# Kernel tuning notes

Hardware: AMD Instinct MI355X
Metric: run time of the kernel (lower is better)

The kernel has to match this reference:

```python
import jax, jax.numpy as jnp
import numpy as np

N_STATES = 35
EMIT_SCALE = -500.0


def _constants():
    prior = jnp.full((N_STATES,), -10.0, dtype=jnp.float32).at[0].set(10.0)
    eye = jnp.eye(N_STATES, dtype=jnp.float32)
    trans = (0.1 * eye
             + 0.8 * jnp.roll(eye, 1, axis=1)
             + 0.08 * jnp.roll(eye, 2, axis=1)
             + (0.02 / N_STATES) * jnp.ones((N_STATES, N_STATES), dtype=jnp.float32))
    # Categorical(probs=trans).logits == log of row-normalized probs
    log_trans = jnp.log(trans / trans.sum(axis=-1, keepdims=True))
    return prior, log_trans


def setup_inputs() -> dict:
    key = jax.random.key(0)
    k1, k2 = jax.random.split(key)
    observations = jax.random.normal(k1, (64, 512, 16, 13, 12), dtype=jnp.float32)
    obs_matrix = jax.random.uniform(k2, (35, 16, 13, 12), dtype=jnp.float32)
    return {"observations": observations, "obs_matrix": obs_matrix}


def reference(observations, obs_matrix):
    prior, log_trans = _constants()
    B, T = observations.shape[:2]
    D = 16 * 13 * 12  # flattened frame dim = 2496
    x = observations.reshape(B, T, D)           # [B,T,D]
    m = obs_matrix.reshape(N_STATES, D)         # [S,D]
    x_sq = jnp.sum(x * x, axis=-1)              # [B,T]
    m_sq = jnp.sum(m * m, axis=-1)              # [S]
    xm = jnp.einsum('btd,sd->bts', x, m)        # [B,T,S]
    emis = (x_sq[..., None] + m_sq[None, None, :] - 2.0 * xm) / EMIT_SCALE  # [B,T,S]

    alpha0 = emis[:, 0] + prior                 # [B,S]
    log_trans_T = log_trans.T                   # [j,i] -> logT[i,j]

    def step(alpha, e_t):
        # alpha'[b,j] = e_t[b,j] + LSE_i(logT[i,j] + alpha[b,i])
        new = e_t + jax.nn.logsumexp(log_trans_T[None, :, :] + alpha[:, None, :], axis=2)
        return new, None

    emis_rest = jnp.swapaxes(emis[:, 1:], 0, 1)  # [T-1,B,S]
    alpha, _ = jax.lax.scan(step, alpha0, emis_rest)
    return jax.nn.logsumexp(alpha, axis=1)       # [B]
```

## Files before the change

### kernel.cpp

```cpp
#include <hip/hip_runtime.h>


#define ROWS 32768
#define KD   2496
#define NS   35
#define SPAD 48
#define ES   40
#define TT   512

typedef short v8s __attribute__((ext_vector_type(8)));
typedef float v4f __attribute__((ext_vector_type(4)));

__device__ __forceinline__ unsigned short f2bf(float f) {
    unsigned u = __builtin_bit_cast(unsigned, f);
    u += 0x7fffu + ((u >> 16) & 1u);
    return (unsigned short)(u >> 16);
}

template <int CTRL, int RM>
__device__ __forceinline__ float dppf(float oldv, float v) {
    return __builtin_bit_cast(float, __builtin_amdgcn_update_dpp(
        __builtin_bit_cast(int, oldv), __builtin_bit_cast(int, v),
        CTRL, RM, 0xf, false));
}

__device__ __forceinline__ float wsum63(float v) {
    v += dppf<0x111, 0xf>(0.f, v);
    v += dppf<0x112, 0xf>(0.f, v);
    v += dppf<0x114, 0xf>(0.f, v);
    v += dppf<0x118, 0xf>(0.f, v);
    v += dppf<0x142, 0xa>(0.f, v);
    v += dppf<0x143, 0xc>(0.f, v);
    return __builtin_bit_cast(float,
        __builtin_amdgcn_readlane(__builtin_bit_cast(int, v), 63));
}

__device__ __forceinline__ float wmax63(float v) {
    const float NI = -3.0e38f;
    v = fmaxf(v, dppf<0x111, 0xf>(NI, v));
    v = fmaxf(v, dppf<0x112, 0xf>(NI, v));
    v = fmaxf(v, dppf<0x114, 0xf>(NI, v));
    v = fmaxf(v, dppf<0x118, 0xf>(NI, v));
    v = fmaxf(v, dppf<0x142, 0xa>(NI, v));
    v = fmaxf(v, dppf<0x143, 0xc>(NI, v));
    return __builtin_bit_cast(float,
        __builtin_amdgcn_readlane(__builtin_bit_cast(int, v), 63));
}

__global__ __launch_bounds__(256) void prep_kernel(
        const float* __restrict__ m, unsigned short* __restrict__ mb,
        float* __restrict__ msq) {
    int s = blockIdx.x;
    int tid = threadIdx.x;
    float part = 0.f;
    for (int k = tid; k < KD; k += 256) {
        float v = (s < NS) ? m[s * KD + k] : 0.f;
        mb[s * KD + k] = f2bf(v);
        part += v * v;
    }
    __shared__ float red[256];
    red[tid] = part;
    __syncthreads();
    for (int off = 128; off > 0; off >>= 1) {
        if (tid < off) red[tid] += red[tid + off];
        __syncthreads();
    }
    if (tid == 0) msq[s] = red[0];
}

__global__ __launch_bounds__(256) void emis_kernel(
        const float* __restrict__ x, const unsigned short* __restrict__ mb,
        const float* __restrict__ msq, float* __restrict__ emis) {
    const int tid = threadIdx.x;
    const int lane = tid & 63, w = tid >> 6;
    const int fm = lane & 15, q = lane >> 4;
    const int row0 = blockIdx.x * 64 + w * 16;
    const float* xr = x + (long)(row0 + fm) * KD + q * 8;
    const unsigned short* mb0 = mb + (long)fm * KD + q * 8;

    v4f acc[3] = {};
    float sq = 0.f;

    float4 cur[6][2], nxt[6][2];
#pragma unroll
    for (int i = 0; i < 6; ++i) {
        cur[i][0] = *(const float4*)&xr[i * 32];
        cur[i][1] = *(const float4*)&xr[i * 32 + 4];
    }
    v8s bc[3], bn[3];
#pragma unroll
    for (int nt = 0; nt < 3; ++nt)
        bc[nt] = *(const v8s*)&mb0[nt * 16 * KD];

    for (int g = 0; g < 13; ++g) {
        const int kbase = g * 192;
        if (g + 1 < 13) {
            const float* xn = xr + kbase + 192;
#pragma unroll
            for (int i = 0; i < 6; ++i) {
                nxt[i][0] = *(const float4*)&xn[i * 32];
                nxt[i][1] = *(const float4*)&xn[i * 32 + 4];
            }
        }
#pragma unroll
        for (int i = 0; i < 6; ++i) {
            const int knext = kbase + (i + 1) * 32;
            if (knext < KD) {
#pragma unroll
                for (int nt = 0; nt < 3; ++nt)
                    bn[nt] = *(const v8s*)&mb0[nt * 16 * KD + knext];
            }
            const float4 v0 = cur[i][0], v1 = cur[i][1];
            sq += v0.x * v0.x + v0.y * v0.y + v0.z * v0.z + v0.w * v0.w
                + v1.x * v1.x + v1.y * v1.y + v1.z * v1.z + v1.w * v1.w;
            v8s a;
            a[0] = (short)f2bf(v0.x); a[1] = (short)f2bf(v0.y);
            a[2] = (short)f2bf(v0.z); a[3] = (short)f2bf(v0.w);
            a[4] = (short)f2bf(v1.x); a[5] = (short)f2bf(v1.y);
            a[6] = (short)f2bf(v1.z); a[7] = (short)f2bf(v1.w);
#pragma unroll
            for (int nt = 0; nt < 3; ++nt)
                acc[nt] = __builtin_amdgcn_mfma_f32_16x16x32_bf16(a, bc[nt], acc[nt], 0, 0, 0);
#pragma unroll
            for (int nt = 0; nt < 3; ++nt) bc[nt] = bn[nt];
        }
#pragma unroll
        for (int i = 0; i < 6; ++i) {
            cur[i][0] = nxt[i][0];
            cur[i][1] = nxt[i][1];
        }
    }

    float s2 = sq + __shfl_xor(sq, 16, 64);
    s2 += __shfl_xor(s2, 32, 64);
    float xs[4];
#pragma unroll
    for (int rg = 0; rg < 4; ++rg)
        xs[rg] = __shfl(s2, q * 4 + rg, 64);

#pragma unroll
    for (int nt = 0; nt < 3; ++nt) {
        const int st = nt * 16 + fm;
        if (st < NS) {
            const float ms = msq[st];
#pragma unroll
            for (int rg = 0; rg < 4; ++rg) {
                emis[(long)(row0 + q * 4 + rg) * ES + st] =
                    (xs[rg] + ms - 2.f * acc[nt][rg]) * (-1.f / 500.f);
            }
        }
    }
}

__global__ __launch_bounds__(64) void forward_kernel(
        const float* __restrict__ emis, float* __restrict__ out) {
    const int b = blockIdx.x;
    const int j = threadIdx.x;
    const bool act = j < NS;
    const int jc = act ? j : NS - 1;
    const float LOG2E = 1.4426950408889634f, LN2 = 0.6931471805599453f;
    const float c0 = 0.1f, c1 = 0.8f, c2 = 0.08f, cb = 0.02f / 35.f;
    const float NI = -3.0e38f;

    const float* ebj = emis + (long)b * TT * ES + jc;
    const int s1 = (j + 34) % 35, s2 = (j + 33) % 35;

    const float e0 = ebj[0];
    const float a0 = (act ? e0 : NI) + ((j == 0) ? 10.f : -10.f);
    float C = wmax63(act ? a0 : NI);
    float p = act ? __builtin_amdgcn_exp2f((a0 - C) * LOG2E) : 0.f;

    float cur[8], nxt[8];
#pragma unroll
    for (int i = 0; i < 8; ++i) cur[i] = ebj[(1 + i) * ES];

    for (int g = 0; g < 63; ++g) {
        const int tb = 9 + 8 * g;
#pragma unroll
        for (int i = 0; i < 8; ++i) {
            const int t = tb + i;
            nxt[i] = ebj[(t < TT ? t : TT - 1) * ES];
        }
        float S = 1.f;
#pragma unroll
        for (int i = 0; i < 8; ++i) {
            const float e = cur[i];
            const float mx = wmax63(act ? e : NI);
            const float E = act ? __builtin_amdgcn_exp2f((e - mx) * LOG2E) : 0.f;
            const float pm1 = __shfl(p, s1, 64);
            const float pm2 = __shfl(p, s2, 64);
            S = wsum63(p);
            const float u = fmaf(c1, pm1, c2 * pm2);
            const float v = fmaf(c0, p, cb * S);
            p = E * (u + v);
            C += mx;
        }
        p *= 1.f / S;
        C += LN2 * __builtin_amdgcn_logf(S);
#pragma unroll
        for (int i = 0; i < 8; ++i) cur[i] = nxt[i];
    }
#pragma unroll
    for (int i = 0; i < 7; ++i) {
        const float e = cur[i];
        const float mx = wmax63(act ? e : NI);
        const float E = act ? __builtin_amdgcn_exp2f((e - mx) * LOG2E) : 0.f;
        const float pm1 = __shfl(p, s1, 64);
        const float pm2 = __shfl(p, s2, 64);
        const float S = wsum63(p);
        const float u = fmaf(c1, pm1, c2 * pm2);
        const float v = fmaf(c0, p, cb * S);
        p = E * (u + v);
        C += mx;
    }
    const float Sf = wsum63(p);
    if (j == 0) out[b] = C + LN2 * __builtin_amdgcn_logf(Sf);
}

extern "C" void kernel_launch(void* const* d_in, const int* in_sizes, int n_in,
                              void* d_out, int out_size, void* d_ws, size_t ws_size,
                              hipStream_t stream) {
    const float* obs  = (const float*)d_in[0];
    const float* obsm = (const float*)d_in[1];
    float* out = (float*)d_out;

    char* ws = (char*)d_ws;
    float* emis = (float*)ws;
    unsigned short* mb = (unsigned short*)(ws + 5242880);
    float* msq = (float*)(ws + 5482496);

    prep_kernel<<<SPAD, 256, 0, stream>>>(obsm, mb, msq);
    emis_kernel<<<ROWS / 64, 256, 0, stream>>>(obs, mb, msq, emis);
    forward_kernel<<<64, 64, 0, stream>>>(emis, out);
}
```

Before: 521.9 us.

## Shorten forward recurrence critical path with group max, DPP shifts, packed bf16 convert

The serial forward recursion now takes one wave-wide max per group of eight timesteps instead of one per step. All exponentials for the group are computed up front, and the per-step normalizer is folded into a single scaled offset. The neighbour-state gathers move from ds_bpermute shuffles to DPP wave shifts plus readlane fixups for the wraparound lanes, and the normalizer reciprocal uses rcp. The emission GEMM converts fp32 to bf16 with the packed v_cvt_pk_bf16_f32 instruction instead of manual rounding. Using one max per group relies on emission values within a group staying close enough to avoid exp underflow or overflow.

```diff
diff --git a/kernel.cpp b/kernel.cpp
--- a/kernel.cpp
+++ b/kernel.cpp
@@ -47,6 +47,21 @@
         __builtin_amdgcn_readlane(__builtin_bit_cast(int, v), 63));
 }
 
+__device__ __forceinline__ float rlane(float v, int l) {
+    return __builtin_bit_cast(float,
+        __builtin_amdgcn_readlane(__builtin_bit_cast(int, v), l));
+}
+
+__device__ __forceinline__ float shr1(float v) {
+    return dppf<0x138, 0xf>(v, v);
+}
+
+__device__ __forceinline__ int cvtpk(float lo, float hi) {
+    int r;
+    asm("v_cvt_pk_bf16_f32 %0, %1, %2" : "=v"(r) : "v"(lo), "v"(hi));
+    return r;
+}
+
 __global__ __launch_bounds__(256) void prep_kernel(
         const float* __restrict__ m, unsigned short* __restrict__ mb,
         float* __restrict__ msq) {
@@ -113,11 +128,12 @@
             const float4 v0 = cur[i][0], v1 = cur[i][1];
             sq += v0.x * v0.x + v0.y * v0.y + v0.z * v0.z + v0.w * v0.w
                 + v1.x * v1.x + v1.y * v1.y + v1.z * v1.z + v1.w * v1.w;
-            v8s a;
-            a[0] = (short)f2bf(v0.x); a[1] = (short)f2bf(v0.y);
-            a[2] = (short)f2bf(v0.z); a[3] = (short)f2bf(v0.w);
-            a[4] = (short)f2bf(v1.x); a[5] = (short)f2bf(v1.y);
-            a[6] = (short)f2bf(v1.z); a[7] = (short)f2bf(v1.w);
+            union { int i4[4]; v8s v; } au;
+            au.i4[0] = cvtpk(v0.x, v0.y);
+            au.i4[1] = cvtpk(v0.z, v0.w);
+            au.i4[2] = cvtpk(v1.x, v1.y);
+            au.i4[3] = cvtpk(v1.z, v1.w);
+            const v8s a = au.v;
 #pragma unroll
             for (int nt = 0; nt < 3; ++nt)
                 acc[nt] = __builtin_amdgcn_mfma_f32_16x16x32_bf16(a, bc[nt], acc[nt], 0, 0, 0);
@@ -157,13 +173,13 @@
     const int b = blockIdx.x;
     const int j = threadIdx.x;
     const bool act = j < NS;
+    const bool is0 = (j == 0), is1 = (j == 1);
     const int jc = act ? j : NS - 1;
     const float LOG2E = 1.4426950408889634f, LN2 = 0.6931471805599453f;
     const float c0 = 0.1f, c1 = 0.8f, c2 = 0.08f, cb = 0.02f / 35.f;
     const float NI = -3.0e38f;
 
     const float* ebj = emis + (long)b * TT * ES + jc;
-    const int s1 = (j + 34) % 35, s2 = (j + 33) % 35;
 
     const float e0 = ebj[0];
     const float a0 = (act ? e0 : NI) + ((j == 0) ? 10.f : -10.f);
@@ -181,38 +197,51 @@
             const int t = tb + i;
             nxt[i] = ebj[(t < TT ? t : TT - 1) * ES];
         }
+        float mx8 = cur[0];
+#pragma unroll
+        for (int i = 1; i < 8; ++i) mx8 = fmaxf(mx8, cur[i]);
+        const float Kg = wmax63(act ? mx8 : NI);
+        float E[8], Eb[8];
+#pragma unroll
+        for (int i = 0; i < 8; ++i) {
+            E[i]  = act ? __builtin_amdgcn_exp2f((cur[i] - Kg) * LOG2E) : 0.f;
+            Eb[i] = E[i] * cb;
+        }
         float S = 1.f;
 #pragma unroll
         for (int i = 0; i < 8; ++i) {
-            const float e = cur[i];
-            const float mx = wmax63(act ? e : NI);
-            const float E = act ? __builtin_amdgcn_exp2f((e - mx) * LOG2E) : 0.f;
-            const float pm1 = __shfl(p, s1, 64);
-            const float pm2 = __shfl(p, s2, 64);
+            const float r1 = shr1(p);
+            const float r2 = shr1(r1);
+            const float p34 = rlane(p, 34), p33 = rlane(p, 33);
+            const float pm1 = is0 ? p34 : r1;
+            const float pm2 = is0 ? p33 : (is1 ? p34 : r2);
             S = wsum63(p);
-            const float u = fmaf(c1, pm1, c2 * pm2);
-            const float v = fmaf(c0, p, cb * S);
-            p = E * (u + v);
-            C += mx;
-        }
-        p *= 1.f / S;
-        C += LN2 * __builtin_amdgcn_logf(S);
+            const float wv = E[i] * fmaf(c1, pm1, fmaf(c2, pm2, c0 * p));
+            p = fmaf(Eb[i], S, wv);
+        }
+        p *= __builtin_amdgcn_rcpf(S);
+        C += 8.f * Kg + LN2 * __builtin_amdgcn_logf(S);
 #pragma unroll
         for (int i = 0; i < 8; ++i) cur[i] = nxt[i];
     }
+    float mx7 = cur[0];
+#pragma unroll
+    for (int i = 1; i < 7; ++i) mx7 = fmaxf(mx7, cur[i]);
+    const float Kt = wmax63(act ? mx7 : NI);
 #pragma unroll
     for (int i = 0; i < 7; ++i) {
-        const float e = cur[i];
-        const float mx = wmax63(act ? e : NI);
-        const float E = act ? __builtin_amdgcn_exp2f((e - mx) * LOG2E) : 0.f;
-        const float pm1 = __shfl(p, s1, 64);
-        const float pm2 = __shfl(p, s2, 64);
+        const float E  = act ? __builtin_amdgcn_exp2f((cur[i] - Kt) * LOG2E) : 0.f;
+        const float Eb = E * cb;
+        const float r1 = shr1(p);
+        const float r2 = shr1(r1);
+        const float p34 = rlane(p, 34), p33 = rlane(p, 33);
+        const float pm1 = is0 ? p34 : r1;
+        const float pm2 = is0 ? p33 : (is1 ? p34 : r2);
         const float S = wsum63(p);
-        const float u = fmaf(c1, pm1, c2 * pm2);
-        const float v = fmaf(c0, p, cb * S);
-        p = E * (u + v);
-        C += mx;
-    }
+        const float wv = E * fmaf(c1, pm1, fmaf(c2, pm2, c0 * p));
+        p = fmaf(Eb, S, wv);
+    }
+    C += 7.f * Kt;
     const float Sf = wsum63(p);
     if (j == 0) out[b] = C + LN2 * __builtin_amdgcn_logf(Sf);
 }
```

Measured after the change: 493.5 us. 5.5% less time.
